# Performance work log

Hardware: AMD Instinct MI355X
Metric: run time of the kernel (lower is better)

Reference implementation:

```python
import jax, jax.numpy as jnp
import numpy as np

ALPHA = 1.0

def setup_inputs() -> dict:
    key = jax.random.key(0)
    k1, k2 = jax.random.split(key)
    x = jax.random.normal(k1, (65536, 512), dtype=jnp.float32)
    clusters = jax.random.normal(k2, (256, 512), dtype=jnp.float32)
    return {"x": x, "clusters": clusters}

def reference(x, clusters):
    # Squared Euclidean distance to each centroid via the GEMM expansion
    x2 = jnp.sum(x * x, axis=1, keepdims=True)            # (B, 1)
    c2 = jnp.sum(clusters * clusters, axis=1)             # (K,)
    cross = x @ clusters.T                                # (B, K) GEMM
    d2 = jnp.maximum(x2 + c2 - 2.0 * cross, 0.0)          # (B, K)
    # Student-t kernel (DEC soft assignment)
    q = 1.0 / (1.0 + d2 / ALPHA)
    q = q ** ((ALPHA + 1.0) / 2.0)
    q = q / jnp.sum(q, axis=1, keepdims=True)             # row-normalize
    return q
```

## Files before the change

kernel.cpp:

```cpp
#include <hip/hip_runtime.h>
#include <hip/hip_bf16.h>


typedef __attribute__((ext_vector_type(8))) short short8v;
typedef __attribute__((ext_vector_type(4))) float f32x4;

#define DDIM 512
#define KCL  256
#define BM   64
#define NT   512
#define BTILE 8192

__device__ __forceinline__ short f2bf(float f) {
    __hip_bfloat16 h = __float2bfloat16(f);
    return __builtin_bit_cast(short, h);
}

__global__ void prep(const float* __restrict__ cl, short* __restrict__ wsB,
                     float* __restrict__ wsC2) {
    const int t = threadIdx.x;
    if (blockIdx.x < 64) {
        const int u = blockIdx.x * 256 + t;
        const int img = u >> 10, gi = u & 1023;
        const int g = gi >> 6, lq = (gi >> 4) & 3, l15 = gi & 15;
        const float* src = cl + (size_t)(g * 16 + l15) * DDIM + img * 32 + lq * 8;
        float4 a = *(const float4*)src;
        float4 b = *(const float4*)(src + 4);
        short8v s;
        s[0]=f2bf(a.x); s[1]=f2bf(a.y); s[2]=f2bf(a.z); s[3]=f2bf(a.w);
        s[4]=f2bf(b.x); s[5]=f2bf(b.y); s[6]=f2bf(b.z); s[7]=f2bf(b.w);
        *(short8v*)&wsB[(size_t)u * 8] = s;
    } else {
        const int cidx = (blockIdx.x - 64) * 16 + (t >> 4);
        const int j = t & 15;
        const float* src = cl + (size_t)cidx * DDIM + j * 32;
        float s = 0.f;
#pragma unroll
        for (int i = 0; i < 8; ++i) {
            float4 v = ((const float4*)src)[i];
            s += v.x*v.x + v.y*v.y + v.z*v.z + v.w*v.w;
        }
        s += __shfl_xor(s, 1); s += __shfl_xor(s, 2);
        s += __shfl_xor(s, 4); s += __shfl_xor(s, 8);
        if (j == 0) wsC2[cidx] = s;
    }
}

#define BAR() asm volatile("s_waitcnt lgkmcnt(0)\ns_barrier" ::: "memory")

__global__ __launch_bounds__(NT, 4)
void dec_main(const float* __restrict__ x, const short* __restrict__ wsB,
              const float* __restrict__ wsC2, float* __restrict__ out) {
    __shared__ __align__(16) short lA[32768];
    __shared__ float s_x2p[2][BM];
    __shared__ float s_rs[4][BM];

    const int t = threadIdx.x, lane = t & 63, w = t >> 6;
    const int rg = w >> 2, cg = w & 3;
    const int l15 = lane & 15, lq = lane >> 4;
    const int row0 = blockIdx.x * BM;

    const int srowS = (w & 3) * 16 + l15;
    const int scolS = (w >> 2) * 32 + lq * 8;
    const float* xs = x + (size_t)(row0 + srowS) * DDIM + scolS;

    const short* bb = wsB + (size_t)(cg * 4) * 512 + (size_t)lane * 8;

    float x2p = 0.f;

    float4 G0a = *(const float4*)(xs +   0), G0b = *(const float4*)(xs +   4);
    float4 G1a = *(const float4*)(xs +  64), G1b = *(const float4*)(xs +  68);
    float4 G2a = *(const float4*)(xs + 128), G2b = *(const float4*)(xs + 132);
    float4 G3a = *(const float4*)(xs + 192), G3b = *(const float4*)(xs + 196);
    float4 G4a = *(const float4*)(xs + 256), G4b = *(const float4*)(xs + 260);
    float4 G5a = *(const float4*)(xs + 320), G5b = *(const float4*)(xs + 324);
    float4 G6a = *(const float4*)(xs + 384), G6b = *(const float4*)(xs + 388);
    float4 G7a = *(const float4*)(xs + 448), G7b = *(const float4*)(xs + 452);

    short8v Ba[4], Bb[4];
#define LOADB(TT, S)                                         \
    {  const short* bt = bb + (size_t)(TT) * BTILE;          \
       S[0] = *(const short8v*)(bt);                         \
       S[1] = *(const short8v*)(bt + 512);                   \
       S[2] = *(const short8v*)(bt + 1024);                  \
       S[3] = *(const short8v*)(bt + 1536); }

    LOADB(0, Ba);

#define STG(CP, GA, GB)                                                          \
    {  short8v s;                                                                \
       s[0]=f2bf(GA.x); s[1]=f2bf(GA.y); s[2]=f2bf(GA.z); s[3]=f2bf(GA.w);       \
       s[4]=f2bf(GB.x); s[5]=f2bf(GB.y); s[6]=f2bf(GB.z); s[7]=f2bf(GB.w);       \
       x2p += GA.x*GA.x + GA.y*GA.y + GA.z*GA.z + GA.w*GA.w                      \
            + GB.x*GB.x + GB.y*GB.y + GB.z*GB.z + GB.w*GB.w;                     \
       *(short8v*)&lA[(CP) * 4096 + t * 8] = s; }

    STG(0, G0a, G0b); STG(1, G1a, G1b); STG(2, G2a, G2b); STG(3, G3a, G3b);
    STG(4, G4a, G4b); STG(5, G5a, G5b); STG(6, G6a, G6b); STG(7, G7a, G7b);

    x2p += __shfl_xor(x2p, 16); x2p += __shfl_xor(x2p, 32);
    if (lane < 16) s_x2p[w >> 2][(w & 3) * 16 + lane] = x2p;

    BAR();

    f32x4 acc[2][4];
#pragma unroll
    for (int m = 0; m < 2; ++m)
#pragma unroll
        for (int n = 0; n < 4; ++n) acc[m][n] = (f32x4){0.f,0.f,0.f,0.f};

    const short* aB = &lA[rg * 1024 + lane * 8];

#define BODY(KK, SU, SN)                                                         \
    {  if ((KK) + 1 < 16) LOADB((KK) + 1, SN);                                   \
       short8v a0 = *(const short8v*)&aB[(KK) * 2048];                           \
       short8v a1 = *(const short8v*)&aB[(KK) * 2048 + 512];                     \
       acc[0][0] = __builtin_amdgcn_mfma_f32_16x16x32_bf16(a0, SU[0], acc[0][0], 0,0,0); \
       acc[0][1] = __builtin_amdgcn_mfma_f32_16x16x32_bf16(a0, SU[1], acc[0][1], 0,0,0); \
       acc[0][2] = __builtin_amdgcn_mfma_f32_16x16x32_bf16(a0, SU[2], acc[0][2], 0,0,0); \
       acc[0][3] = __builtin_amdgcn_mfma_f32_16x16x32_bf16(a0, SU[3], acc[0][3], 0,0,0); \
       acc[1][0] = __builtin_amdgcn_mfma_f32_16x16x32_bf16(a1, SU[0], acc[1][0], 0,0,0); \
       acc[1][1] = __builtin_amdgcn_mfma_f32_16x16x32_bf16(a1, SU[1], acc[1][1], 0,0,0); \
       acc[1][2] = __builtin_amdgcn_mfma_f32_16x16x32_bf16(a1, SU[2], acc[1][2], 0,0,0); \
       acc[1][3] = __builtin_amdgcn_mfma_f32_16x16x32_bf16(a1, SU[3], acc[1][3], 0,0,0); }

    BODY( 0, Ba, Bb); BODY( 1, Bb, Ba); BODY( 2, Ba, Bb); BODY( 3, Bb, Ba);
    BODY( 4, Ba, Bb); BODY( 5, Bb, Ba); BODY( 6, Ba, Bb); BODY( 7, Bb, Ba);
    BODY( 8, Ba, Bb); BODY( 9, Bb, Ba); BODY(10, Ba, Bb); BODY(11, Bb, Ba);
    BODY(12, Ba, Bb); BODY(13, Bb, Ba); BODY(14, Ba, Bb); BODY(15, Bb, Ba);

    float c2a[4];
#pragma unroll
    for (int n = 0; n < 4; ++n) c2a[n] = wsC2[cg*64 + n*16 + l15];

#pragma unroll
    for (int m = 0; m < 2; ++m)
#pragma unroll
        for (int n = 0; n < 4; ++n)
#pragma unroll
            for (int r = 0; r < 4; ++r) {
                const int rw = rg*32 + m*16 + lq*4 + r;
                const float x2v = s_x2p[0][rw] + s_x2p[1][rw];
                float d2 = fmaxf(x2v + c2a[n] - 2.0f * acc[m][n][r], 0.0f);
                acc[m][n][r] = 1.0f / (1.0f + d2);
            }

#pragma unroll
    for (int m = 0; m < 2; ++m)
#pragma unroll
        for (int r = 0; r < 4; ++r) {
            float p = acc[m][0][r] + acc[m][1][r] + acc[m][2][r] + acc[m][3][r];
            p += __shfl_xor(p, 1); p += __shfl_xor(p, 2);
            p += __shfl_xor(p, 4); p += __shfl_xor(p, 8);
            if (l15 == 0) s_rs[cg][rg*32 + m*16 + lq*4 + r] = p;
        }
    __syncthreads();

#pragma unroll
    for (int m = 0; m < 2; ++m)
#pragma unroll
        for (int r = 0; r < 4; ++r) {
            const int rw = rg*32 + m*16 + lq*4 + r;
            const float rinv = 1.0f / (s_rs[0][rw] + s_rs[1][rw] + s_rs[2][rw] + s_rs[3][rw]);
            float* o = out + (size_t)(row0 + rw) * KCL + cg*64 + l15;
#pragma unroll
            for (int n = 0; n < 4; ++n)
                o[n * 16] = acc[m][n][r] * rinv;
        }
}

extern "C" void kernel_launch(void* const* d_in, const int* in_sizes, int n_in,
                              void* d_out, int out_size, void* d_ws, size_t ws_size,
                              hipStream_t stream) {
    const float* x  = (const float*)d_in[0];
    const float* cl = (const float*)d_in[1];
    float* out = (float*)d_out;
    short* wsB  = (short*)d_ws;
    float* wsC2 = (float*)((char*)d_ws + (size_t)16 * BTILE * sizeof(short));

    prep<<<80, 256, 0, stream>>>(cl, wsB, wsC2);
    const int B = in_sizes[0] / DDIM;
    dec_main<<<B / BM, NT, 0, stream>>>(x, wsB, wsC2, out);
}
```

Measured before the change: 61.35 us.

## Process four row tiles per block with double-buffered LDS and prefetched x loads

Each block now handles four 64-row tiles instead of one. The global x loads for the next tile are issued in the middle of the current tile's MFMA loop, and the converted data goes into a second LDS buffer, so memory latency overlaps compute. The B operand is kept in a 4-deep register ring. This amortizes block launch and prologue cost and hides the x fetch latency, in exchange for doubled LDS use (about 128KB per block) and lower occupancy (launch bounds drop from 4 to 2 blocks) with a quarter as many blocks.

```diff
diff --git a/kernel.cpp b/kernel.cpp
--- a/kernel.cpp
+++ b/kernel.cpp
@@ -10,6 +10,7 @@
 #define BM   64
 #define NT   512
 #define BTILE 8192
+#define TPB  4
 
 __device__ __forceinline__ short f2bf(float f) {
     __hip_bfloat16 h = __float2bfloat16(f);
@@ -46,38 +47,35 @@
     }
 }
 
-#define BAR() asm volatile("s_waitcnt lgkmcnt(0)\ns_barrier" ::: "memory")
+#define BAR()    asm volatile("s_waitcnt lgkmcnt(0)\ns_barrier" ::: "memory")
+#define SFENCE() __builtin_amdgcn_sched_barrier(0)
 
-__global__ __launch_bounds__(NT, 4)
+__global__ __launch_bounds__(NT, 2)
 void dec_main(const float* __restrict__ x, const short* __restrict__ wsB,
               const float* __restrict__ wsC2, float* __restrict__ out) {
-    __shared__ __align__(16) short lA[32768];
-    __shared__ float s_x2p[2][BM];
+    __shared__ __align__(16) short lA[2][32768];
+    __shared__ float s_x2p[2][2][BM];
     __shared__ float s_rs[4][BM];
 
     const int t = threadIdx.x, lane = t & 63, w = t >> 6;
     const int rg = w >> 2, cg = w & 3;
     const int l15 = lane & 15, lq = lane >> 4;
-    const int row0 = blockIdx.x * BM;
+    const int row0 = blockIdx.x * (TPB * BM);
 
     const int srowS = (w & 3) * 16 + l15;
     const int scolS = (w >> 2) * 32 + lq * 8;
     const float* xs = x + (size_t)(row0 + srowS) * DDIM + scolS;
-
     const short* bb = wsB + (size_t)(cg * 4) * 512 + (size_t)lane * 8;
 
-    float x2p = 0.f;
+    float c2a[4];
+#pragma unroll
+    for (int n = 0; n < 4; ++n) c2a[n] = wsC2[cg*64 + n*16 + l15];
 
-    float4 G0a = *(const float4*)(xs +   0), G0b = *(const float4*)(xs +   4);
-    float4 G1a = *(const float4*)(xs +  64), G1b = *(const float4*)(xs +  68);
-    float4 G2a = *(const float4*)(xs + 128), G2b = *(const float4*)(xs + 132);
-    float4 G3a = *(const float4*)(xs + 192), G3b = *(const float4*)(xs + 196);
-    float4 G4a = *(const float4*)(xs + 256), G4b = *(const float4*)(xs + 260);
-    float4 G5a = *(const float4*)(xs + 320), G5b = *(const float4*)(xs + 324);
-    float4 G6a = *(const float4*)(xs + 384), G6b = *(const float4*)(xs + 388);
-    float4 G7a = *(const float4*)(xs + 448), G7b = *(const float4*)(xs + 452);
+    f32x4 acc[2][4];
+    float x2p;
+    short8v Ba[4], Bb[4], Bc[4], Bd[4];
+    float4 G0a,G0b,G1a,G1b,G2a,G2b,G3a,G3b,G4a,G4b,G5a,G5b,G6a,G6b,G7a,G7b;
 
-    short8v Ba[4], Bb[4];
 #define LOADB(TT, S)                                         \
     {  const short* bt = bb + (size_t)(TT) * BTILE;          \
        S[0] = *(const short8v*)(bt);                         \
@@ -85,88 +83,94 @@
        S[2] = *(const short8v*)(bt + 1024);                  \
        S[3] = *(const short8v*)(bt + 1536); }
 
-    LOADB(0, Ba);
+#define GISSUE(IT)                                                   \
+    {  const float* xg = xs + (size_t)(IT) * (BM * DDIM);            \
+       G0a = *(const float4*)(xg);       G0b = *(const float4*)(xg + 4);   \
+       G1a = *(const float4*)(xg + 64);  G1b = *(const float4*)(xg + 68);  \
+       G2a = *(const float4*)(xg + 128); G2b = *(const float4*)(xg + 132); \
+       G3a = *(const float4*)(xg + 192); G3b = *(const float4*)(xg + 196); \
+       G4a = *(const float4*)(xg + 256); G4b = *(const float4*)(xg + 260); \
+       G5a = *(const float4*)(xg + 320); G5b = *(const float4*)(xg + 324); \
+       G6a = *(const float4*)(xg + 384); G6b = *(const float4*)(xg + 388); \
+       G7a = *(const float4*)(xg + 448); G7b = *(const float4*)(xg + 452); }
 
-#define STG(CP, GA, GB)                                                          \
-    {  short8v s;                                                                \
-       s[0]=f2bf(GA.x); s[1]=f2bf(GA.y); s[2]=f2bf(GA.z); s[3]=f2bf(GA.w);       \
-       s[4]=f2bf(GB.x); s[5]=f2bf(GB.y); s[6]=f2bf(GB.z); s[7]=f2bf(GB.w);       \
+#define STG1(PARN, CP, GA, GB)                                                   \
+    {  short8v s_;                                                               \
+       s_[0]=f2bf(GA.x); s_[1]=f2bf(GA.y); s_[2]=f2bf(GA.z); s_[3]=f2bf(GA.w);   \
+       s_[4]=f2bf(GB.x); s_[5]=f2bf(GB.y); s_[6]=f2bf(GB.z); s_[7]=f2bf(GB.w);   \
        x2p += GA.x*GA.x + GA.y*GA.y + GA.z*GA.z + GA.w*GA.w                      \
             + GB.x*GB.x + GB.y*GB.y + GB.z*GB.z + GB.w*GB.w;                     \
-       *(short8v*)&lA[(CP) * 4096 + t * 8] = s; }
+       *(short8v*)&lA[PARN][(CP)*4096 + t*8] = s_; }
 
-    STG(0, G0a, G0b); STG(1, G1a, G1b); STG(2, G2a, G2b); STG(3, G3a, G3b);
-    STG(4, G4a, G4b); STG(5, G5a, G5b); STG(6, G6a, G6b); STG(7, G7a, G7b);
+#define CVT(PARN)                                                                \
+    {  x2p = 0.f;                                                                \
+       STG1(PARN,0,G0a,G0b) STG1(PARN,1,G1a,G1b)                                 \
+       STG1(PARN,2,G2a,G2b) STG1(PARN,3,G3a,G3b)                                 \
+       STG1(PARN,4,G4a,G4b) STG1(PARN,5,G5a,G5b)                                 \
+       STG1(PARN,6,G6a,G6b) STG1(PARN,7,G7a,G7b)                                 \
+       x2p += __shfl_xor(x2p,16); x2p += __shfl_xor(x2p,32);                     \
+       if (lane < 16) s_x2p[PARN][w>>2][(w&3)*16 + lane] = x2p; }
 
-    x2p += __shfl_xor(x2p, 16); x2p += __shfl_xor(x2p, 32);
-    if (lane < 16) s_x2p[w >> 2][(w & 3) * 16 + lane] = x2p;
+#define BODY(KK, PAR, SU, RF)                                                    \
+    {  const short* aB_ = &lA[PAR][rg*1024 + lane*8 + (KK)*2048];                \
+       short8v a0_ = *(const short8v*)aB_;                                       \
+       short8v a1_ = *(const short8v*)(aB_ + 512);                               \
+       acc[0][0] = __builtin_amdgcn_mfma_f32_16x16x32_bf16(a0_, SU[0], acc[0][0], 0,0,0); \
+       acc[0][1] = __builtin_amdgcn_mfma_f32_16x16x32_bf16(a0_, SU[1], acc[0][1], 0,0,0); \
+       acc[0][2] = __builtin_amdgcn_mfma_f32_16x16x32_bf16(a0_, SU[2], acc[0][2], 0,0,0); \
+       acc[0][3] = __builtin_amdgcn_mfma_f32_16x16x32_bf16(a0_, SU[3], acc[0][3], 0,0,0); \
+       acc[1][0] = __builtin_amdgcn_mfma_f32_16x16x32_bf16(a1_, SU[0], acc[1][0], 0,0,0); \
+       acc[1][1] = __builtin_amdgcn_mfma_f32_16x16x32_bf16(a1_, SU[1], acc[1][1], 0,0,0); \
+       acc[1][2] = __builtin_amdgcn_mfma_f32_16x16x32_bf16(a1_, SU[2], acc[1][2], 0,0,0); \
+       acc[1][3] = __builtin_amdgcn_mfma_f32_16x16x32_bf16(a1_, SU[3], acc[1][3], 0,0,0); \
+       if (RF) { LOADB(((KK)+4)&15, SU); } }
 
+#define ITER(IT, PAR, PARN)                                                      \
+    {  _Pragma("unroll") for (int m=0;m<2;++m)                                   \
+       _Pragma("unroll") for (int n=0;n<4;++n) acc[m][n]=(f32x4){0.f,0.f,0.f,0.f}; \
+       BODY(0,PAR,Ba,1)  BODY(1,PAR,Bb,1)  BODY(2,PAR,Bc,1)  BODY(3,PAR,Bd,1)    \
+       BODY(4,PAR,Ba,1)  BODY(5,PAR,Bb,1)  BODY(6,PAR,Bc,1)  BODY(7,PAR,Bd,1)    \
+       BODY(8,PAR,Ba,1)  BODY(9,PAR,Bb,1)  BODY(10,PAR,Bc,1) BODY(11,PAR,Bd,1)   \
+       SFENCE();                                                                 \
+       if ((IT) < TPB-1) { GISSUE((IT)+1); }                                     \
+       SFENCE();                                                                 \
+       BODY(12,PAR,Ba,(IT)<TPB-1) BODY(13,PAR,Bb,(IT)<TPB-1)                     \
+       BODY(14,PAR,Bc,(IT)<TPB-1) BODY(15,PAR,Bd,(IT)<TPB-1)                     \
+                        \
+       _Pragma("unroll") for (int m=0;m<2;++m)                                   \
+       _Pragma("unroll") for (int n=0;n<4;++n)                                   \
+       _Pragma("unroll") for (int r=0;r<4;++r) {                                 \
+           const int rw = rg*32 + m*16 + lq*4 + r;                               \
+           const float x2v = s_x2p[PAR][0][rw] + s_x2p[PAR][1][rw];              \
+           float d2 = fmaxf(x2v + c2a[n] - 2.0f*acc[m][n][r], 0.0f);             \
+           acc[m][n][r] = 1.0f/(1.0f + d2); }                                    \
+       _Pragma("unroll") for (int m=0;m<2;++m)                                   \
+       _Pragma("unroll") for (int r=0;r<4;++r) {                                 \
+           float p = acc[m][0][r]+acc[m][1][r]+acc[m][2][r]+acc[m][3][r];        \
+           p += __shfl_xor(p,1); p += __shfl_xor(p,2);                           \
+           p += __shfl_xor(p,4); p += __shfl_xor(p,8);                           \
+           if (l15 == 0) s_rs[cg][rg*32 + m*16 + lq*4 + r] = p; }                \
+       BAR();                                                                    \
+       _Pragma("unroll") for (int m=0;m<2;++m)                                   \
+       _Pragma("unroll") for (int r=0;r<4;++r) {                                 \
+           const int rw = rg*32 + m*16 + lq*4 + r;                               \
+           const float rinv = 1.0f/(s_rs[0][rw]+s_rs[1][rw]+s_rs[2][rw]+s_rs[3][rw]); \
+           float* o = out + (size_t)(row0 + (IT)*BM + rw)*KCL + cg*64 + l15;     \
+           _Pragma("unroll") for (int n=0;n<4;++n) o[n*16] = acc[m][n][r]*rinv; }\
+       if ((IT) < TPB-1) { CVT(PARN); }                                          \
+       BAR(); }
+
+    LOADB(0, Ba); LOADB(1, Bb); LOADB(2, Bc); LOADB(3, Bd);
+    SFENCE();
+    GISSUE(0);
+    SFENCE();
+    CVT(0);
     BAR();
 
-    f32x4 acc[2][4];
-#pragma unroll
-    for (int m = 0; m < 2; ++m)
-#pragma unroll
-        for (int n = 0; n < 4; ++n) acc[m][n] = (f32x4){0.f,0.f,0.f,0.f};
-
-    const short* aB = &lA[rg * 1024 + lane * 8];
-
-#define BODY(KK, SU, SN)                                                         \
-    {  if ((KK) + 1 < 16) LOADB((KK) + 1, SN);                                   \
-       short8v a0 = *(const short8v*)&aB[(KK) * 2048];                           \
-       short8v a1 = *(const short8v*)&aB[(KK) * 2048 + 512];                     \
-       acc[0][0] = __builtin_amdgcn_mfma_f32_16x16x32_bf16(a0, SU[0], acc[0][0], 0,0,0); \
-       acc[0][1] = __builtin_amdgcn_mfma_f32_16x16x32_bf16(a0, SU[1], acc[0][1], 0,0,0); \
-       acc[0][2] = __builtin_amdgcn_mfma_f32_16x16x32_bf16(a0, SU[2], acc[0][2], 0,0,0); \
-       acc[0][3] = __builtin_amdgcn_mfma_f32_16x16x32_bf16(a0, SU[3], acc[0][3], 0,0,0); \
-       acc[1][0] = __builtin_amdgcn_mfma_f32_16x16x32_bf16(a1, SU[0], acc[1][0], 0,0,0); \
-       acc[1][1] = __builtin_amdgcn_mfma_f32_16x16x32_bf16(a1, SU[1], acc[1][1], 0,0,0); \
-       acc[1][2] = __builtin_amdgcn_mfma_f32_16x16x32_bf16(a1, SU[2], acc[1][2], 0,0,0); \
-       acc[1][3] = __builtin_amdgcn_mfma_f32_16x16x32_bf16(a1, SU[3], acc[1][3], 0,0,0); }
-
-    BODY( 0, Ba, Bb); BODY( 1, Bb, Ba); BODY( 2, Ba, Bb); BODY( 3, Bb, Ba);
-    BODY( 4, Ba, Bb); BODY( 5, Bb, Ba); BODY( 6, Ba, Bb); BODY( 7, Bb, Ba);
-    BODY( 8, Ba, Bb); BODY( 9, Bb, Ba); BODY(10, Ba, Bb); BODY(11, Bb, Ba);
-    BODY(12, Ba, Bb); BODY(13, Bb, Ba); BODY(14, Ba, Bb); BODY(15, Bb, Ba);
-
-    float c2a[4];
-#pragma unroll
-    for (int n = 0; n < 4; ++n) c2a[n] = wsC2[cg*64 + n*16 + l15];
-
-#pragma unroll
-    for (int m = 0; m < 2; ++m)
-#pragma unroll
-        for (int n = 0; n < 4; ++n)
-#pragma unroll
-            for (int r = 0; r < 4; ++r) {
-                const int rw = rg*32 + m*16 + lq*4 + r;
-                const float x2v = s_x2p[0][rw] + s_x2p[1][rw];
-                float d2 = fmaxf(x2v + c2a[n] - 2.0f * acc[m][n][r], 0.0f);
-                acc[m][n][r] = 1.0f / (1.0f + d2);
-            }
-
-#pragma unroll
-    for (int m = 0; m < 2; ++m)
-#pragma unroll
-        for (int r = 0; r < 4; ++r) {
-            float p = acc[m][0][r] + acc[m][1][r] + acc[m][2][r] + acc[m][3][r];
-            p += __shfl_xor(p, 1); p += __shfl_xor(p, 2);
-            p += __shfl_xor(p, 4); p += __shfl_xor(p, 8);
-            if (l15 == 0) s_rs[cg][rg*32 + m*16 + lq*4 + r] = p;
-        }
-    __syncthreads();
-
-#pragma unroll
-    for (int m = 0; m < 2; ++m)
-#pragma unroll
-        for (int r = 0; r < 4; ++r) {
-            const int rw = rg*32 + m*16 + lq*4 + r;
-            const float rinv = 1.0f / (s_rs[0][rw] + s_rs[1][rw] + s_rs[2][rw] + s_rs[3][rw]);
-            float* o = out + (size_t)(row0 + rw) * KCL + cg*64 + l15;
-#pragma unroll
-            for (int n = 0; n < 4; ++n)
-                o[n * 16] = acc[m][n][r] * rinv;
-        }
+    ITER(0, 0, 1)
+    ITER(1, 1, 0)
+    ITER(2, 0, 1)
+    ITER(3, 1, 0)
 }
 
 extern "C" void kernel_launch(void* const* d_in, const int* in_sizes, int n_in,
@@ -180,5 +184,5 @@
 
     prep<<<80, 256, 0, stream>>>(cl, wsB, wsC2);
     const int B = in_sizes[0] / DDIM;
-    dec_main<<<B / BM, NT, 0, stream>>>(x, wsB, wsC2, out);
+    dec_main<<<B / (BM * TPB), NT, 0, stream>>>(x, wsB, wsC2, out);
 }
```

Result: slower. 97.99 us (+59.7%).
